# Kernel tuning notes

Hardware: AMD Instinct MI355X
Metric: run time of the kernel (lower is better)

## Reference

```python
import jax, jax.numpy as jnp
import numpy as np

B, N, D = 16, 2048, 1024   # batch, num_windows, input_dim
H, A = 256, 128            # feature head dim, attention hidden dim
EPS = 1e-5                 # torch LayerNorm eps
NEG = -1e9                 # finite mask value (avoids NaN in softmax/grads)
KMAX = max(1, N // 10)     # static upper bound on per-sample top-k


def setup_inputs() -> dict:
    key = jax.random.key(0)
    ks = jax.random.split(key, 6)
    rn = lambda k, shape, sc: jax.random.normal(k, shape, jnp.float32) * sc
    return {
        "x": rn(ks[0], (B, N, D), 1.0),
        "lengths": jax.random.randint(ks[1], (B,), 0, N, dtype=jnp.int64)
                   if jax.config.jax_enable_x64 else
                   jax.random.randint(ks[1], (B,), 0, N, dtype=jnp.int32),
        # feature_head: Linear(D,H) + LayerNorm(H) (+ GELU, dropout=eval no-op)
        "W1": rn(ks[2], (H, D), D ** -0.5), "b1": jnp.zeros((H,), jnp.float32),
        "ln_g": jnp.ones((H,), jnp.float32), "ln_b": jnp.zeros((H,), jnp.float32),
        # attention: Linear(H,A) -> tanh -> Linear(A,1)
        "Wa1": rn(ks[3], (A, H), H ** -0.5), "ba1": jnp.zeros((A,), jnp.float32),
        "Wa2": rn(ks[4], (1, A), A ** -0.5), "ba2": jnp.zeros((1,), jnp.float32),
        # classifier: Linear(H,1)
        "Wc": rn(ks[5], (1, H), H ** -0.5), "bc": jnp.zeros((1,), jnp.float32),
    }


def reference(x, lengths, W1, b1, ln_g, ln_b, Wa1, ba1, Wa2, ba2, Wc, bc):
    # feature head: Linear + LayerNorm + exact GELU (dropout is identity in eval)
    h = jnp.einsum('bnd,hd->bnh', x, W1) + b1
    mu = h.mean(-1, keepdims=True)
    var = h.var(-1, keepdims=True)  # biased, as in torch LayerNorm
    h = (h - mu) * jax.lax.rsqrt(var + EPS) * ln_g + ln_b
    h = jax.nn.gelu(h, approximate=False)

    instance_scores = jnp.einsum('bnh,oh->bno', h, Wc)[..., 0] + bc[0]   # (B, N)
    a_hidden = jnp.tanh(jnp.einsum('bnh,ah->bna', h, Wa1) + ba1)
    attn_logits = jnp.einsum('bna,oa->bno', a_hidden, Wa2)[..., 0] + ba2[0]  # (B, N)

    T = lengths                                    # (B,)
    mask = jnp.arange(N)[None, :] < T[:, None]     # (B, N) valid-window mask

    # masked softmax attention pooling over the first T windows
    w = jax.nn.softmax(jnp.where(mask, attn_logits, NEG), axis=1)
    attn_score = jnp.sum(w * instance_scores * mask, axis=1)

    # dynamic top-k: k = max(1, floor(0.1*T)); take static KMAX then mask ranks
    k_i = jnp.maximum(1, T // 10)                  # (B,)
    vals, _ = jax.lax.top_k(jnp.where(mask, instance_scores, NEG), KMAX)
    rank_mask = jnp.arange(KMAX)[None, :] < k_i[:, None]
    topk_mean = jnp.sum(vals * rank_mask, axis=1) / k_i.astype(vals.dtype)

    video = jnp.where(T > 0, 0.5 * attn_score + 0.5 * topk_mean,
                      jnp.zeros((), vals.dtype))
    return video[:, None], instance_scores
```

## Files before the change

### kernel.cpp

```cpp
#include <hip/hip_runtime.h>
#include <hip/hip_bf16.h>
#include <cmath>

#define Bn 16
#define Nn 2048
#define Dn 1024
#define Hn 256
#define An 128

typedef __bf16 bf16x8 __attribute__((ext_vector_type(8)));
typedef float f32x4 __attribute__((ext_vector_type(4)));
typedef unsigned short ushort8v __attribute__((ext_vector_type(8)));
typedef unsigned int uint4v __attribute__((ext_vector_type(4)));

#define LDS_BARRIER do {                                   \
    asm volatile("s_waitcnt lgkmcnt(0)" ::: "memory");     \
    __builtin_amdgcn_s_barrier();                          \
    __builtin_amdgcn_sched_barrier(0);                     \
  } while (0)

static __device__ __forceinline__ unsigned short f2bf(float f) {
  unsigned u = __float_as_uint(f);
  u += 0x7fffu + ((u >> 16) & 1u);
  return (unsigned short)(u >> 16);
}

static __device__ __forceinline__ bf16x8 cvt8(const float4 a, const float4 b) {
  bf16x8 r;
  r[0] = (__bf16)a.x; r[1] = (__bf16)a.y; r[2] = (__bf16)a.z; r[3] = (__bf16)a.w;
  r[4] = (__bf16)b.x; r[5] = (__bf16)b.y; r[6] = (__bf16)b.z; r[7] = (__bf16)b.w;
  return r;
}

__global__ __launch_bounds__(256) void pack_weights(
    const float* __restrict__ W1, const float* __restrict__ Wa1,
    unsigned short* __restrict__ w1p, unsigned short* __restrict__ wa1p) {
  const int idx = blockIdx.x * 256 + threadIdx.x;
  const float* src;
  unsigned short* dst;
  if (blockIdx.x < 128) {
    const int kc  = idx >> 10;
    const int u   = idx & 1023;
    const int col = u >> 2;
    const int lq  = (u & 3) ^ ((col >> 1) & 3);
    src = W1 + (size_t)col * Dn + (kc << 5) + (lq << 3);
    dst = w1p + (size_t)idx * 8;
  } else {
    const int v   = idx - 32768;
    const int row = v >> 5;
    const int ls  = (v & 31) ^ (row & 7);
    src = Wa1 + (size_t)row * Hn + (ls << 3);
    dst = wa1p + (size_t)v * 8;
  }
  const float4 a = *(const float4*)src;
  const float4 b = *(const float4*)(src + 4);
  ushort8v o;
  o[0] = f2bf(a.x); o[1] = f2bf(a.y); o[2] = f2bf(a.z); o[3] = f2bf(a.w);
  o[4] = f2bf(b.x); o[5] = f2bf(b.y); o[6] = f2bf(b.z); o[7] = f2bf(b.w);
  *(ushort8v*)dst = o;
}

#define K1A(p) ((p) * 16384)
#define K1H    0
#define K1RED  32768
__global__ __launch_bounds__(256, 2) void gemm_ln_kernel(
    const float* __restrict__ x,
    const float* __restrict__ b1,
    const float* __restrict__ ln_g,
    const float* __restrict__ ln_b,
    const float* __restrict__ Wc,
    const float* __restrict__ bc,
    const unsigned short* __restrict__ w1p,
    float* __restrict__ scores_out,
    unsigned short* __restrict__ h_out)
{
  __shared__ __align__(16) char lds[34816];

  const int tid  = threadIdx.x;
  const int wv   = tid >> 6;
  const int lane = tid & 63;
  const int l15  = lane & 15;
  const int lhi  = lane >> 4;
  const int rg   = wv >> 1;
  const int cw   = wv & 1;

  const int gr0 = blockIdx.x << 6;
  const int bb  = gr0 >> 11;
  const int n0  = gr0 & (Nn - 1);

  f32x4 acc[2][8];
  #pragma unroll
  for (int rf = 0; rf < 2; ++rf)
    #pragma unroll
    for (int cf = 0; cf < 8; ++cf)
      acc[rf][cf] = (f32x4){0.f, 0.f, 0.f, 0.f};

  const int arow = tid >> 2, akq = tid & 3;
  const float* xsrc = x + (size_t)(gr0 + arow) * Dn + (akq << 5);

  const int ar0 = (rg << 5) + l15;
  const int ar1 = ar0 + 16;
  const int axk = l15 & 7;

  const int pq = lhi ^ ((l15 >> 1) & 3);
  const unsigned short* bbase = w1p + (size_t)(((cw << 7) + l15) << 5) + (pq << 3);

  float4 ast[8];
  bf16x8 Bpre[2][8];

  auto loadA = [&](int ch) {
    #pragma unroll
    for (int j = 0; j < 8; ++j)
      ast[j] = *(const float4*)(xsrc + (ch << 7) + (j << 2));
  };
  auto writeA = [&](int p) {
    #pragma unroll
    for (int j = 0; j < 4; ++j)
      *(bf16x8*)(lds + K1A(p) + arow * 256 +
                 ((((akq << 2) + j) ^ (arow & 7)) << 4)) = cvt8(ast[2 * j], ast[2 * j + 1]);
  };
  auto loadB = [&](bf16x8* dst, int kc) {
    #pragma unroll
    for (int cf = 0; cf < 8; ++cf)
      dst[cf] = *(const bf16x8*)(bbase + (size_t)kc * 8192 + (cf << 9));
  };
  auto computeStep = [&](const bf16x8* Bf, int p, int s) {
    const char* Ab = lds + K1A(p);
    const int sx = ((((s << 2) + lhi) ^ axk) << 4);
    const bf16x8 a0 = *(const bf16x8*)(Ab + ar0 * 256 + sx);
    const bf16x8 a1 = *(const bf16x8*)(Ab + ar1 * 256 + sx);
    __builtin_amdgcn_s_setprio(1);
    #pragma unroll
    for (int cf = 0; cf < 8; ++cf) {
      acc[0][cf] = __builtin_amdgcn_mfma_f32_16x16x32_bf16(a0, Bf[cf], acc[0][cf], 0, 0, 0);
      acc[1][cf] = __builtin_amdgcn_mfma_f32_16x16x32_bf16(a1, Bf[cf], acc[1][cf], 0, 0, 0);
    }
    __builtin_amdgcn_s_setprio(0);
  };

  loadA(0);
  writeA(0);
  loadB(Bpre[0], 0);
  loadB(Bpre[1], 1);
  LDS_BARRIER;
  loadA(1);

  #pragma unroll
  for (int kc = 0; kc < 32; ++kc) {
    const int s  = kc & 3;
    const int cb = (kc >> 2) & 1;
    computeStep(Bpre[kc & 1], cb, s);
    if (kc < 30) loadB(Bpre[kc & 1], kc + 2);
    if (s == 3 && kc < 31) {
      writeA(cb ^ 1);
      LDS_BARRIER;
      if ((kc >> 2) < 6) loadA((kc >> 2) + 2);
    }
  }
  __syncthreads();

  float (*red)[8] = (float(*)[8])(lds + K1RED);

  const float bc0 = bc[0];
  float b1v[8];
  #pragma unroll
  for (int cf = 0; cf < 8; ++cf) b1v[cf] = b1[(cw << 7) + (cf << 4) + l15];

  float ps[2][4], ps2[2][4];
  #pragma unroll
  for (int rf = 0; rf < 2; ++rf)
    #pragma unroll
    for (int r = 0; r < 4; ++r) { ps[rf][r] = 0.f; ps2[rf][r] = 0.f; }

  #pragma unroll
  for (int rf = 0; rf < 2; ++rf)
    #pragma unroll
    for (int cf = 0; cf < 8; ++cf)
      #pragma unroll
      for (int r = 0; r < 4; ++r) {
        const float v = acc[rf][cf][r] + b1v[cf];
        acc[rf][cf][r] = v;
        ps[rf][r] += v; ps2[rf][r] += v * v;
      }
  #pragma unroll
  for (int rf = 0; rf < 2; ++rf)
    #pragma unroll
    for (int r = 0; r < 4; ++r)
      #pragma unroll
      for (int s = 1; s < 16; s <<= 1) {
        ps[rf][r]  += __shfl_xor(ps[rf][r],  s, 64);
        ps2[rf][r] += __shfl_xor(ps2[rf][r], s, 64);
      }
  if (l15 == 0) {
    #pragma unroll
    for (int rf = 0; rf < 2; ++rf)
      #pragma unroll
      for (int r = 0; r < 4; ++r) {
        const int rowb = (rg << 5) + (rf << 4) + (lhi << 2) + r;
        red[rowb][cw << 1]       = ps[rf][r];
        red[rowb][(cw << 1) + 1] = ps2[rf][r];
      }
  }
  __syncthreads();

  float mu[2][4], inv[2][4];
  #pragma unroll
  for (int rf = 0; rf < 2; ++rf)
    #pragma unroll
    for (int r = 0; r < 4; ++r) {
      const int rowb = (rg << 5) + (rf << 4) + (lhi << 2) + r;
      const float s = red[rowb][0] + red[rowb][2];
      const float q = red[rowb][1] + red[rowb][3];
      const float m = s * (1.f / 256.f);
      const float var = q * (1.f / 256.f) - m * m;
      mu[rf][r] = m;
      inv[rf][r] = rsqrtf(var + 1e-5f);
    }

  float gv[8], bv[8], wcv[8];
  #pragma unroll
  for (int cf = 0; cf < 8; ++cf) {
    const int col = (cw << 7) + (cf << 4) + l15;
    gv[cf] = ln_g[col]; bv[cf] = ln_b[col]; wcv[cf] = Wc[col];
  }
  float sc[2][4];
  #pragma unroll
  for (int rf = 0; rf < 2; ++rf)
    #pragma unroll
    for (int r = 0; r < 4; ++r) sc[rf][r] = 0.f;

  #pragma unroll
  for (int rf = 0; rf < 2; ++rf)
    #pragma unroll
    for (int cf = 0; cf < 8; ++cf)
      #pragma unroll
      for (int r = 0; r < 4; ++r) {
        float v = (acc[rf][cf][r] - mu[rf][r]) * inv[rf][r] * gv[cf] + bv[cf];
        v = 0.5f * v * (1.f + erff(v * 0.70710678118654752f));
        sc[rf][r] += v * wcv[cf];
        const int rowb = (rg << 5) + (rf << 4) + (lhi << 2) + r;
        const int col  = (cw << 7) + (cf << 4) + l15;
        *(__bf16*)(lds + K1H + rowb * 512 + (((col >> 3) ^ (rowb & 7)) << 4)
                   + ((col & 7) << 1)) = (__bf16)v;
      }
  #pragma unroll
  for (int rf = 0; rf < 2; ++rf)
    #pragma unroll
    for (int r = 0; r < 4; ++r)
      #pragma unroll
      for (int s = 1; s < 16; s <<= 1)
        sc[rf][r] += __shfl_xor(sc[rf][r], s, 64);
  if (l15 == 0) {
    #pragma unroll
    for (int rf = 0; rf < 2; ++rf)
      #pragma unroll
      for (int r = 0; r < 4; ++r) {
        const int rowb = (rg << 5) + (rf << 4) + (lhi << 2) + r;
        red[rowb][4 + cw] = sc[rf][r];
      }
  }
  __syncthreads();
  if (tid < 64)
    scores_out[(size_t)bb * Nn + n0 + tid] = red[tid][4] + red[tid][5] + bc0;

  #pragma unroll
  for (int j = 0; j < 8; ++j) {
    const int g   = (j << 8) + tid;
    const int row = g >> 5;
    const int c   = g & 31;
    const bf16x8 hv = *(const bf16x8*)(lds + K1H + row * 512 +
                                       ((c ^ (row & 7)) << 4));
    *(bf16x8*)(h_out + (size_t)(gr0 + row) * 256 + (c << 3)) = hv;
  }
}

__global__ __launch_bounds__(512) void stage2_kernel(
    const unsigned short* __restrict__ h_in,
    const unsigned short* __restrict__ wa1p,
    const float* __restrict__ ba1,
    const float* __restrict__ Wa2,
    const float* __restrict__ ba2,
    float* __restrict__ logits_out)
{
  __shared__ __align__(16) char lds2[65536];

  const int tid  = threadIdx.x;
  const int wv   = tid >> 6;
  const int lane = tid & 63;
  const int l15  = lane & 15;
  const int lhi  = lane >> 4;

  const int gr0 = blockIdx.x << 7;
  const int bb  = gr0 >> 11;
  const int n0  = gr0 & (Nn - 1);

  {
    uint4v st[8];
    #pragma unroll
    for (int j = 0; j < 8; ++j)
      st[j] = *(const uint4v*)(wa1p + (size_t)((j << 9) + tid) * 8);
    #pragma unroll
    for (int j = 0; j < 8; ++j)
      *(uint4v*)(lds2 + ((j << 9) + tid) * 16) = st[j];
  }
  __syncthreads();

  f32x4 acc2[8];
  #pragma unroll
  for (int cf = 0; cf < 8; ++cf) acc2[cf] = (f32x4){0.f, 0.f, 0.f, 0.f};

  const unsigned short* hrow = h_in + (size_t)(gr0 + (wv << 4) + l15) * 256 + (lhi << 3);
  #pragma unroll
  for (int ks = 0; ks < 8; ++ks) {
    const bf16x8 af = *(const bf16x8*)(hrow + (ks << 5));
    #pragma unroll
    for (int cf = 0; cf < 8; ++cf) {
      const int row2 = (cf << 4) + l15;
      const bf16x8 bfr = *(const bf16x8*)(lds2 + row2 * 512 +
                          ((((ks << 2) + lhi) ^ (row2 & 7)) << 4));
      acc2[cf] = __builtin_amdgcn_mfma_f32_16x16x32_bf16(af, bfr, acc2[cf], 0, 0, 0);
    }
  }
  const float ba20 = ba2[0];
  float lg[4] = {0.f, 0.f, 0.f, 0.f};
  #pragma unroll
  for (int cf = 0; cf < 8; ++cf) {
    const int col = (cf << 4) + l15;
    const float bav = ba1[col], w2v = Wa2[col];
    #pragma unroll
    for (int r = 0; r < 4; ++r) {
      const float t = acc2[cf][r] + bav;
      const float e = __expf(2.f * t);
      const float th = 1.f - 2.f / (e + 1.f);
      lg[r] += th * w2v;
    }
  }
  #pragma unroll
  for (int r = 0; r < 4; ++r)
    #pragma unroll
    for (int s = 1; s < 16; s <<= 1) lg[r] += __shfl_xor(lg[r], s, 64);
  if (l15 == 0) {
    #pragma unroll
    for (int r = 0; r < 4; ++r)
      logits_out[(size_t)bb * Nn + n0 + (wv << 4) + (lhi << 2) + r] = lg[r] + ba20;
  }
}

__global__ __launch_bounds__(256) void finalize_kernel(
    const int* __restrict__ lengths,
    const float* __restrict__ scores,
    const float* __restrict__ logits,
    float* __restrict__ video)
{
  const int b = blockIdx.x;
  const int tid = threadIdx.x;
  __shared__ float sS[Nn];
  __shared__ float sL[Nn];
  __shared__ unsigned skey[Nn];
  __shared__ float sred[8];

  const int T = lengths[b];
  for (int i = tid; i < Nn; i += 256) {
    sS[i] = scores[(size_t)b * Nn + i];
    sL[i] = logits[(size_t)b * Nn + i];
  }
  __syncthreads();
  if (T <= 0) { if (tid == 0) video[b] = 0.f; return; }

  float m = -3.0e38f;
  for (int i = tid; i < T; i += 256) m = fmaxf(m, sL[i]);
  #pragma unroll
  for (int s = 1; s < 64; s <<= 1) m = fmaxf(m, __shfl_xor(m, s, 64));
  if ((tid & 63) == 0) sred[tid >> 6] = m;
  __syncthreads();
  m = fmaxf(fmaxf(sred[0], sred[1]), fmaxf(sred[2], sred[3]));
  __syncthreads();

  float se = 0.f, swe = 0.f;
  for (int i = tid; i < T; i += 256) {
    const float e = expf(sL[i] - m);
    se += e; swe += e * sS[i];
  }
  #pragma unroll
  for (int s = 1; s < 64; s <<= 1) { se += __shfl_xor(se, s, 64); swe += __shfl_xor(swe, s, 64); }
  if ((tid & 63) == 0) { sred[tid >> 6] = se; sred[4 + (tid >> 6)] = swe; }
  __syncthreads();
  se  = sred[0] + sred[1] + sred[2] + sred[3];
  swe = sred[4] + sred[5] + sred[6] + sred[7];
  __syncthreads();
  const float attn = swe / se;

  for (int i = tid; i < T; i += 256) {
    const unsigned u = __float_as_uint(sS[i]);
    skey[i] = (u & 0x80000000u) ? ~u : (u | 0x80000000u);
  }
  __syncthreads();
  const int k = max(1, T / 10);
  unsigned ans = 0u;
  for (int bit = 31; bit >= 0; --bit) {
    const unsigned cand = ans | (1u << bit);
    int c = 0;
    for (int i = tid; i < T; i += 256) c += (skey[i] >= cand) ? 1 : 0;
    #pragma unroll
    for (int s = 1; s < 64; s <<= 1) c += __shfl_xor(c, s, 64);
    if ((tid & 63) == 0) sred[tid >> 6] = (float)c;
    __syncthreads();
    c = (int)(sred[0] + sred[1] + sred[2] + sred[3]);
    __syncthreads();
    if (c >= k) ans = cand;
  }
  int cgt = 0; float sgt = 0.f;
  for (int i = tid; i < T; i += 256) {
    if (skey[i] > ans) { cgt++; sgt += sS[i]; }
  }
  #pragma unroll
  for (int s = 1; s < 64; s <<= 1) { cgt += __shfl_xor(cgt, s, 64); sgt += __shfl_xor(sgt, s, 64); }
  if ((tid & 63) == 0) { sred[tid >> 6] = (float)cgt; sred[4 + (tid >> 6)] = sgt; }
  __syncthreads();
  cgt = (int)(sred[0] + sred[1] + sred[2] + sred[3]);
  sgt = sred[4] + sred[5] + sred[6] + sred[7];

  const unsigned ub = (ans & 0x80000000u) ? (ans ^ 0x80000000u) : ~ans;
  const float kth = __uint_as_float(ub);
  const float topk = (sgt + (float)(k - cgt) * kth) / (float)k;
  if (tid == 0) video[b] = 0.5f * attn + 0.5f * topk;
}

extern "C" void kernel_launch(void* const* d_in, const int* in_sizes, int n_in,
                              void* d_out, int out_size, void* d_ws, size_t ws_size,
                              hipStream_t stream) {
  const float* x    = (const float*)d_in[0];
  const int*   len  = (const int*)  d_in[1];
  const float* W1   = (const float*)d_in[2];
  const float* b1   = (const float*)d_in[3];
  const float* ln_g = (const float*)d_in[4];
  const float* ln_b = (const float*)d_in[5];
  const float* Wa1  = (const float*)d_in[6];
  const float* ba1  = (const float*)d_in[7];
  const float* Wa2  = (const float*)d_in[8];
  const float* ba2  = (const float*)d_in[9];
  const float* Wc   = (const float*)d_in[10];
  const float* bc   = (const float*)d_in[11];

  float* out    = (float*)d_out;
  float* video  = out;
  float* scores = out + Bn;

  char* ws = (char*)d_ws;
  float*          logits = (float*)ws;
  unsigned short* h_g    = (unsigned short*)(ws + 131072);
  unsigned short* w1p    = (unsigned short*)(ws + 131072 + 16777216);
  unsigned short* wa1p   = (unsigned short*)(ws + 131072 + 16777216 + 524288);

  hipLaunchKernelGGL(pack_weights, dim3(144), dim3(256), 0, stream, W1, Wa1, w1p, wa1p);
  hipLaunchKernelGGL(gemm_ln_kernel, dim3(Bn * Nn / 64), dim3(256), 0, stream,
                     x, b1, ln_g, ln_b, Wc, bc, w1p, scores, h_g);
  hipLaunchKernelGGL(stage2_kernel, dim3(Bn * Nn / 128), dim3(512), 0, stream,
                     h_g, wa1p, ba1, Wa2, ba2, logits);
  hipLaunchKernelGGL(finalize_kernel, dim3(Bn), dim3(256), 0, stream, len, scores, logits, video);
}
```

Baseline: 97.51 us.

## Load A operand directly from global into registers, bypassing LDS staging

The GEMM main loop no longer stages the fp32 x tile through LDS with barriers. Each lane now loads its own A fragment straight from global memory into a two-slot register double buffer and converts it to bf16 just before the MFMAs. This removes the LDS writes, LDS reads and block barriers. In exchange, the two column-wave pairs each load the same x rows, doubling global/L2 traffic for A, and the per-lane loads are less coalesced.

```diff
diff --git a/kernel.cpp b/kernel.cpp
--- a/kernel.cpp
+++ b/kernel.cpp
@@ -12,12 +12,6 @@
 typedef float f32x4 __attribute__((ext_vector_type(4)));
 typedef unsigned short ushort8v __attribute__((ext_vector_type(8)));
 typedef unsigned int uint4v __attribute__((ext_vector_type(4)));
-
-#define LDS_BARRIER do {                                   \
-    asm volatile("s_waitcnt lgkmcnt(0)" ::: "memory");     \
-    __builtin_amdgcn_s_barrier();                          \
-    __builtin_amdgcn_sched_barrier(0);                     \
-  } while (0)
 
 static __device__ __forceinline__ unsigned short f2bf(float f) {
   unsigned u = __float_as_uint(f);
@@ -60,7 +54,6 @@
   *(ushort8v*)dst = o;
 }
 
-#define K1A(p) ((p) * 16384)
 #define K1H    0
 #define K1RED  32768
 __global__ __launch_bounds__(256, 2) void gemm_ln_kernel(
@@ -95,67 +88,44 @@
     for (int cf = 0; cf < 8; ++cf)
       acc[rf][cf] = (f32x4){0.f, 0.f, 0.f, 0.f};
 
-  const int arow = tid >> 2, akq = tid & 3;
-  const float* xsrc = x + (size_t)(gr0 + arow) * Dn + (akq << 5);
-
-  const int ar0 = (rg << 5) + l15;
-  const int ar1 = ar0 + 16;
-  const int axk = l15 & 7;
+  const float* xA = x + (size_t)(gr0 + (rg << 5) + l15) * Dn + (lhi << 3);
 
   const int pq = lhi ^ ((l15 >> 1) & 3);
-  const unsigned short* bbase = w1p + (size_t)(((cw << 7) + l15) << 5) + (pq << 3);
-
-  float4 ast[8];
-  bf16x8 Bpre[2][8];
-
-  auto loadA = [&](int ch) {
-    #pragma unroll
-    for (int j = 0; j < 8; ++j)
-      ast[j] = *(const float4*)(xsrc + (ch << 7) + (j << 2));
+  const unsigned short* bbase = w1p + (((cw << 7) + l15) << 5) + (pq << 3);
+
+  float4 Ax[2][4];
+  bf16x8 Bp[2][8];
+
+  auto loadSlot = [&](int sl, int kc) {
+    const float* ap = xA + (kc << 5);
+    Ax[sl][0] = *(const float4*)(ap);
+    Ax[sl][1] = *(const float4*)(ap + 4);
+    Ax[sl][2] = *(const float4*)(ap + (size_t)16 * Dn);
+    Ax[sl][3] = *(const float4*)(ap + (size_t)16 * Dn + 4);
+    const unsigned short* bp = bbase + (size_t)kc * 8192;
+    #pragma unroll
+    for (int cf = 0; cf < 8; ++cf)
+      Bp[sl][cf] = *(const bf16x8*)(bp + (cf << 9));
   };
-  auto writeA = [&](int p) {
-    #pragma unroll
-    for (int j = 0; j < 4; ++j)
-      *(bf16x8*)(lds + K1A(p) + arow * 256 +
-                 ((((akq << 2) + j) ^ (arow & 7)) << 4)) = cvt8(ast[2 * j], ast[2 * j + 1]);
-  };
-  auto loadB = [&](bf16x8* dst, int kc) {
-    #pragma unroll
-    for (int cf = 0; cf < 8; ++cf)
-      dst[cf] = *(const bf16x8*)(bbase + (size_t)kc * 8192 + (cf << 9));
-  };
-  auto computeStep = [&](const bf16x8* Bf, int p, int s) {
-    const char* Ab = lds + K1A(p);
-    const int sx = ((((s << 2) + lhi) ^ axk) << 4);
-    const bf16x8 a0 = *(const bf16x8*)(Ab + ar0 * 256 + sx);
-    const bf16x8 a1 = *(const bf16x8*)(Ab + ar1 * 256 + sx);
+  auto step = [&](int sl) {
+    const bf16x8 a0 = cvt8(Ax[sl][0], Ax[sl][1]);
+    const bf16x8 a1 = cvt8(Ax[sl][2], Ax[sl][3]);
     __builtin_amdgcn_s_setprio(1);
     #pragma unroll
     for (int cf = 0; cf < 8; ++cf) {
-      acc[0][cf] = __builtin_amdgcn_mfma_f32_16x16x32_bf16(a0, Bf[cf], acc[0][cf], 0, 0, 0);
-      acc[1][cf] = __builtin_amdgcn_mfma_f32_16x16x32_bf16(a1, Bf[cf], acc[1][cf], 0, 0, 0);
+      acc[0][cf] = __builtin_amdgcn_mfma_f32_16x16x32_bf16(a0, Bp[sl][cf], acc[0][cf], 0, 0, 0);
+      acc[1][cf] = __builtin_amdgcn_mfma_f32_16x16x32_bf16(a1, Bp[sl][cf], acc[1][cf], 0, 0, 0);
     }
     __builtin_amdgcn_s_setprio(0);
   };
 
-  loadA(0);
-  writeA(0);
-  loadB(Bpre[0], 0);
-  loadB(Bpre[1], 1);
-  LDS_BARRIER;
-  loadA(1);
+  loadSlot(0, 0);
+  loadSlot(1, 1);
 
   #pragma unroll
   for (int kc = 0; kc < 32; ++kc) {
-    const int s  = kc & 3;
-    const int cb = (kc >> 2) & 1;
-    computeStep(Bpre[kc & 1], cb, s);
-    if (kc < 30) loadB(Bpre[kc & 1], kc + 2);
-    if (s == 3 && kc < 31) {
-      writeA(cb ^ 1);
-      LDS_BARRIER;
-      if ((kc >> 2) < 6) loadA((kc >> 2) + 2);
-    }
+    step(kc & 1);
+    if (kc < 30) loadSlot(kc & 1, kc + 2);
   }
   __syncthreads();
 
```

Result: slower. 104.9 us (+7.5%).
